# Optimization experiments

Hardware: AMD Instinct MI355X
Metric: run time of the kernel (lower is better)

Reference implementation:

```python
import jax, jax.numpy as jnp
import numpy as np

B, N, C, H = 4, 8192, 1024, 16
D = C // H

def setup_inputs() -> dict:
    key = jax.random.key(0)
    k1, k2, k3 = jax.random.split(key, 3)
    scale_in = 1.0 / np.sqrt(C)
    return {
        "x": jax.random.normal(k1, (B, N, C), dtype=jnp.float32),
        "w_qkv": jax.random.normal(k2, (C, 3 * C), dtype=jnp.float32) * scale_in,
        "b_qkv": jnp.zeros((3 * C,), dtype=jnp.float32),
        "w_proj": jax.random.normal(k3, (C, C), dtype=jnp.float32) * scale_in,
        "b_proj": jnp.zeros((C,), dtype=jnp.float32),
    }

def reference(x, w_qkv, b_qkv, w_proj, b_proj):
    Bx, Nx, Cx = x.shape
    qkv = x @ w_qkv + b_qkv                       # [B,N,3C]
    qkv = qkv.reshape(Bx, Nx, 3, H, D)
    qkv = jnp.transpose(qkv, (2, 0, 3, 1, 4))     # [3,B,H,N,D]
    q, k, v = qkv[0], qkv[1], qkv[2]
    q = jax.nn.elu(q) + 1.0                       # positive feature map
    k = jax.nn.elu(k) + 1.0
    kv = jnp.einsum('bhnd,bhne->bhde', k, v)      # [B,H,D,D]
    out = jnp.einsum('bhnd,bhde->bhne', q, kv)    # [B,H,N,D]
    z = 1.0 / (jnp.einsum('bhnd,bhd->bhn', q, k.sum(axis=2)) + 1e-8)
    out = out * z[..., None]
    out = jnp.transpose(out, (0, 2, 1, 3)).reshape(Bx, Nx, Cx)
    out = out @ w_proj + b_proj                   # dropout is identity in eval
    return out
```

## Files before the change

kernel.cpp:

```cpp
#include <hip/hip_runtime.h>
#include <hip/hip_bf16.h>
#include <stdint.h>

typedef unsigned short ushort_t;
typedef __attribute__((ext_vector_type(8))) short short8;
typedef __attribute__((ext_vector_type(4))) float floatx4;

__device__ __forceinline__ ushort_t f2b(float f) {
    unsigned u = __float_as_uint(f);
    unsigned r = (u + 0x7FFFu + ((u >> 16) & 1u)) >> 16;
    return (ushort_t)r;
}
__device__ __forceinline__ float b2f(ushort_t h) {
    return __uint_as_float(((unsigned)h) << 16);
}
__device__ __forceinline__ float elu1(float f) {
    return (f > 0.f) ? (f + 1.f) : __expf(f);
}

#define GLDS16(srcp, dstp)                                                          \
    __builtin_amdgcn_global_load_lds(                                               \
        (const __attribute__((address_space(1))) unsigned int*)(srcp),              \
        (__attribute__((address_space(3))) unsigned int*)(dstp), 16, 0, 0)


__global__ void conv_bf16(const float* __restrict__ in, ushort_t* __restrict__ out, int n8) {
    for (int i = blockIdx.x * blockDim.x + threadIdx.x; i < n8; i += gridDim.x * blockDim.x) {
        const float4 f0 = *(const float4*)&in[(size_t)i * 8];
        const float4 f1 = *(const float4*)&in[(size_t)i * 8 + 4];
        ushort4 o0, o1;
        o0.x = f2b(f0.x); o0.y = f2b(f0.y); o0.z = f2b(f0.z); o0.w = f2b(f0.w);
        o1.x = f2b(f1.x); o1.y = f2b(f1.y); o1.z = f2b(f1.z); o1.w = f2b(f1.w);
        *(ushort4*)&out[(size_t)i * 8]     = o0;
        *(ushort4*)&out[(size_t)i * 8 + 4] = o1;
    }
}

__global__ void transpose_conv(const float* __restrict__ in, ushort_t* __restrict__ out,
                               int R, int C) {
    __shared__ float tile[32][33];
    int c0 = blockIdx.x * 32, r0 = blockIdx.y * 32;
    int tx = threadIdx.x, ty = threadIdx.y;
#pragma unroll
    for (int k = 0; k < 4; ++k) {
        int a = ty * 4 + k;
        tile[a][tx] = in[(size_t)(r0 + a) * C + c0 + tx];
    }
    __syncthreads();
#pragma unroll
    for (int k = 0; k < 4; ++k) {
        int a = ty * 4 + k;
        out[(size_t)(c0 + a) * R + r0 + tx] = f2b(tile[tx][a]);
    }
}

__global__ void zero_f32(float* __restrict__ p, int n) {
    int i = blockIdx.x * blockDim.x + threadIdx.x;
    if (i < n) p[i] = 0.f;
}

template<int MODE>
__global__ __launch_bounds__(512, 2) void gemm256(
    const ushort_t* __restrict__ A, const ushort_t* __restrict__ Bt,
    const float* __restrict__ bias,
    ushort_t* __restrict__ out_u16, float* __restrict__ out_f32,
    int Nt, int nbx)
{
    extern __shared__ ushort_t lds[];
    constexpr int KK = 1024;

    const int tid  = threadIdx.x;
    const int wave = tid >> 6;
    const int lane = tid & 63;
    const int wm_i = wave >> 2;
    const int wn_i = wave & 3;
    const int fr   = lane & 15;
    const int fq   = lane >> 4;

    const int nwg = (int)gridDim.x;
    const int bid = (int)blockIdx.x;
    const int swz = (bid & 7) * (nwg >> 3) + (bid >> 3);
    const int bx = swz % nbx, by = swz / nbx;
    const int m0 = by * 256, n0 = bx * 256;

    const int trow = tid >> 3;
    const int csw  = ((tid & 7) ^ (trow & 7)) << 3;
    const int tcolB = ((tid >> 8) << 6) + (trow & 31);

    const ushort_t* sa = A  + (size_t)(m0 + trow)  * KK + csw;
    const ushort_t* sb = Bt + (size_t)(n0 + tcolB) * KK + csw;

    const int dstA = wave * 512;
    const int dstB = 16384 + wave * 512;

    const int sw0 = (fq ^ (fr & 7)) << 3;
    const int sw1 = sw0 ^ 32;
    const int abase = (wm_i * 64 + fr) * 64;
    const int bbase = (wn_i * 32 + fr) * 64;
    int loA0[2][2], loA1[2][2], loB0[2][2], loB1[2][2];
#pragma unroll
    for (int bf = 0; bf < 2; ++bf)
#pragma unroll
        for (int q = 0; q < 2; ++q) {
            loA0[bf][q] = bf * 32768 + q * 8192 + abase + sw0;
            loA1[bf][q] = bf * 32768 + q * 8192 + abase + sw1;
            loB0[bf][q] = bf * 32768 + 16384 + q * 8192 + bbase + sw0;
            loB1[bf][q] = bf * 32768 + 16384 + q * 8192 + bbase + sw1;
        }

    floatx4 acc[8][4];
    const floatx4 z4 = {0.f, 0.f, 0.f, 0.f};
#pragma unroll
    for (int i = 0; i < 8; ++i)
#pragma unroll
        for (int j = 0; j < 4; ++j) acc[i][j] = z4;

    short8 a[4][2], b[2][2];

    auto stageA = [&](int buf, int h, int ko) {
        ushort_t* d = lds + buf * 32768 + h * 8192 + dstA;
        GLDS16(sa + h * (64 * KK) + ko, d);
        GLDS16(sa + h * (64 * KK) + 128 * KK + ko, d + 4096);
    };
    auto stageB = [&](int buf, int h, int ko) {
        ushort_t* d = lds + buf * 32768 + h * 8192 + dstB;
        GLDS16(sb + h * (32 * KK) + ko, d);
        GLDS16(sb + h * (32 * KK) + 128 * KK + ko, d + 4096);
    };
    auto loadA = [&](int buf, int qr) {
        const int o0 = loA0[buf][qr], o1 = loA1[buf][qr];
#pragma unroll
        for (int i = 0; i < 4; ++i) {
            a[i][0] = *(const short8*)(lds + o0 + i * 1024);
            a[i][1] = *(const short8*)(lds + o1 + i * 1024);
        }
    };
    auto loadB = [&](int buf, int qc) {
        const int o0 = loB0[buf][qc], o1 = loB1[buf][qc];
#pragma unroll
        for (int j = 0; j < 2; ++j) {
            b[j][0] = *(const short8*)(lds + o0 + j * 1024);
            b[j][1] = *(const short8*)(lds + o1 + j * 1024);
        }
    };
    auto mma = [&](int qr, int qc) {
#pragma unroll
        for (int i = 0; i < 4; ++i)
#pragma unroll
            for (int j = 0; j < 2; ++j) {
                acc[qr * 4 + i][qc * 2 + j] =
                    __builtin_amdgcn_mfma_f32_16x16x32_bf16(b[j][0], a[i][0], acc[qr * 4 + i][qc * 2 + j], 0, 0, 0);
                acc[qr * 4 + i][qc * 2 + j] =
                    __builtin_amdgcn_mfma_f32_16x16x32_bf16(b[j][1], a[i][1], acc[qr * 4 + i][qc * 2 + j], 0, 0, 0);
            }
    };

#define PRIO1() __builtin_amdgcn_s_setprio(1)
#define BOUT()  __builtin_amdgcn_s_setprio(0); __builtin_amdgcn_s_barrier()
#define VM6()   asm volatile("s_waitcnt vmcnt(6)" ::: "memory")
#define VM0()   asm volatile("s_waitcnt vmcnt(0)" ::: "memory")

    stageA(0, 0, 0);
    stageB(0, 1, 0);
    stageA(0, 1, 0);
    stageB(0, 0, 0);
    stageA(1, 0, 64);
    stageB(1, 1, 64);
    stageA(1, 1, 64);
    VM6();
    __builtin_amdgcn_s_barrier();

    int ko = 0;
    for (int pr = 0; pr < 7; ++pr, ko += 128) {
        loadA(0, 0); loadB(0, 0);
        stageB(1, 0, ko + 64);
        PRIO1(); mma(0, 0); BOUT();

        loadB(0, 1);
        stageA(0, 0, ko + 128);
        PRIO1(); mma(0, 1); BOUT();

        loadA(0, 1);
        stageB(0, 1, ko + 128);
        PRIO1(); mma(1, 1); BOUT();

        loadB(0, 0);
        stageA(0, 1, ko + 128);
        PRIO1(); mma(1, 0); __builtin_amdgcn_s_setprio(0); VM6();
        __builtin_amdgcn_s_barrier();

        loadA(1, 0); loadB(1, 0);
        stageB(0, 0, ko + 128);
        PRIO1(); mma(0, 0); BOUT();

        loadB(1, 1);
        stageA(1, 0, ko + 192);
        PRIO1(); mma(0, 1); BOUT();

        loadA(1, 1);
        stageB(1, 1, ko + 192);
        PRIO1(); mma(1, 1); BOUT();

        loadB(1, 0);
        stageA(1, 1, ko + 192);
        PRIO1(); mma(1, 0); __builtin_amdgcn_s_setprio(0); VM6();
        __builtin_amdgcn_s_barrier();
    }

    loadA(0, 0); loadB(0, 0);
    stageB(1, 0, 960);
    PRIO1(); mma(0, 0); BOUT();

    loadB(0, 1);
    PRIO1(); mma(0, 1); BOUT();

    loadA(0, 1);
    PRIO1(); mma(1, 1); BOUT();

    loadB(0, 0);
    PRIO1(); mma(1, 0); __builtin_amdgcn_s_setprio(0); VM0();
    __builtin_amdgcn_s_barrier();

    loadA(1, 0); loadB(1, 0);
    PRIO1(); mma(0, 0); BOUT();

    loadB(1, 1);
    PRIO1(); mma(0, 1); BOUT();

    loadA(1, 1);
    PRIO1(); mma(1, 1); BOUT();

    loadB(1, 0);
    PRIO1(); mma(1, 0);
    __builtin_amdgcn_s_setprio(0);

#undef PRIO1
#undef BOUT
#undef VM6
#undef VM0

    float4 bv[4];
#pragma unroll
    for (int cj = 0; cj < 4; ++cj) {
        const int nb = n0 + wn_i * 64 + (cj >> 1) * 32 + (cj & 1) * 16 + fq * 4;
        bv[cj] = *(const float4*)&bias[nb];
    }
#pragma unroll
    for (int ri = 0; ri < 8; ++ri) {
        const int m = m0 + wm_i * 128 + (ri >> 2) * 64 + (ri & 3) * 16 + fr;
#pragma unroll
        for (int cj = 0; cj < 4; ++cj) {
            const int nb = n0 + wn_i * 64 + (cj >> 1) * 32 + (cj & 1) * 16 + fq * 4;
            if (MODE == 0) {
                ushort4 o;
                o.x = f2b(acc[ri][cj][0] + bv[cj].x);
                o.y = f2b(acc[ri][cj][1] + bv[cj].y);
                o.z = f2b(acc[ri][cj][2] + bv[cj].z);
                o.w = f2b(acc[ri][cj][3] + bv[cj].w);
                *(ushort4*)&out_u16[(size_t)m * Nt + nb] = o;
            } else {
                float4 o;
                o.x = acc[ri][cj][0] + bv[cj].x;
                o.y = acc[ri][cj][1] + bv[cj].y;
                o.z = acc[ri][cj][2] + bv[cj].z;
                o.w = acc[ri][cj][3] + bv[cj].w;
                *(float4*)&out_f32[(size_t)m * Nt + nb] = o;
            }
        }
    }
}

__global__ __launch_bounds__(256) void kv_kernel(
    const ushort_t* __restrict__ qkvb,
    float* __restrict__ kv, float* __restrict__ ksum)
{
    __shared__ ushort_t ks[64 * 64] __attribute__((aligned(16)));
    __shared__ ushort_t vs[64 * 64] __attribute__((aligned(16)));

    const int bh = blockIdx.y, chunk = blockIdx.x, t = threadIdx.x;
    const int b = bh >> 4, h = bh & 15;
    const int d0 = (t >> 4) * 4, e0 = (t & 15) * 4;
    const bool do_ksum = (t & 15) == 0;

    const int sr = t >> 2;
    const int sc = (t & 3) * 16;

    float acc[4][4];
#pragma unroll
    for (int i = 0; i < 4; ++i)
#pragma unroll
        for (int j = 0; j < 4; ++j) acc[i][j] = 0.f;
    float kacc[4] = {0.f, 0.f, 0.f, 0.f};

    for (int sub = 0; sub < 8; ++sub) {
        const int nb = chunk * 512 + sub * 64;
        __syncthreads();
        {
            const ushort_t* row = qkvb + ((size_t)b * 8192 + nb + sr) * 3072 + h * 64 + sc;
            short8 k0 = *(const short8*)(row + 1024);
            short8 k1 = *(const short8*)(row + 1024 + 8);
            short8 ko0, ko1;
#pragma unroll
            for (int i = 0; i < 8; ++i) {
                ko0[i] = (short)f2b(elu1(b2f((ushort_t)k0[i])));
                ko1[i] = (short)f2b(elu1(b2f((ushort_t)k1[i])));
            }
            *(short8*)&ks[sr * 64 + sc]     = ko0;
            *(short8*)&ks[sr * 64 + sc + 8] = ko1;
            *(short8*)&vs[sr * 64 + sc]     = *(const short8*)(row + 2048);
            *(short8*)&vs[sr * 64 + sc + 8] = *(const short8*)(row + 2048 + 8);
        }
        __syncthreads();
        for (int n = 0; n < 64; ++n) {
            ushort4 kd = *(const ushort4*)&ks[n * 64 + d0];
            ushort4 ve = *(const ushort4*)&vs[n * 64 + e0];
            float kf[4] = {b2f(kd.x), b2f(kd.y), b2f(kd.z), b2f(kd.w)};
            float vf[4] = {b2f(ve.x), b2f(ve.y), b2f(ve.z), b2f(ve.w)};
#pragma unroll
            for (int i = 0; i < 4; ++i) {
#pragma unroll
                for (int j = 0; j < 4; ++j) acc[i][j] += kf[i] * vf[j];
            }
            if (do_ksum) {
#pragma unroll
                for (int i = 0; i < 4; ++i) kacc[i] += kf[i];
            }
        }
    }
#pragma unroll
    for (int i = 0; i < 4; ++i) {
        if (do_ksum) atomicAdd(&ksum[bh * 64 + d0 + i], kacc[i]);
#pragma unroll
        for (int j = 0; j < 4; ++j)
            atomicAdd(&kv[((size_t)bh * 64 + d0 + i) * 64 + e0 + j], acc[i][j]);
    }
}

__global__ __launch_bounds__(256) void out_kernel(
    const ushort_t* __restrict__ qkvb, const float* __restrict__ kv,
    const float* __restrict__ ksum, ushort_t* __restrict__ obuf)
{
    __shared__ float kvs[4096];
    __shared__ float ksums[64];
    __shared__ float qs[16][65];

    const int bh = blockIdx.y, chunk = blockIdx.x, t = threadIdx.x;
    const int b = bh >> 4, h = bh & 15;
    const int myrow = t >> 4, e0 = (t & 15) * 4;

#pragma unroll
    for (int i = 0; i < 4; ++i) {
        int idx = (i * 256 + t) * 4;
        *(float4*)&kvs[idx] = *(const float4*)&kv[(size_t)bh * 4096 + idx];
    }
    if (t < 64) ksums[t] = ksum[bh * 64 + t];

    for (int pass = 0; pass < 8; ++pass) {
        const int n = chunk * 128 + pass * 16 + myrow;
        __syncthreads();
        {
            int col = (t & 15) * 4;
            ushort4 qv4 = *(const ushort4*)&qkvb[((size_t)b * 8192 + n) * 3072 + h * 64 + col];
            qs[myrow][col + 0] = elu1(b2f(qv4.x));
            qs[myrow][col + 1] = elu1(b2f(qv4.y));
            qs[myrow][col + 2] = elu1(b2f(qv4.z));
            qs[myrow][col + 3] = elu1(b2f(qv4.w));
        }
        __syncthreads();
        float a0 = 0.f, a1 = 0.f, a2 = 0.f, a3 = 0.f, z = 0.f;
        for (int d = 0; d < 64; ++d) {
            const float qv = qs[myrow][d];
            const float4 kvv = *(const float4*)&kvs[d * 64 + e0];
            a0 += qv * kvv.x; a1 += qv * kvv.y; a2 += qv * kvv.z; a3 += qv * kvv.w;
            z += qv * ksums[d];
        }
        const float zi = 1.f / (z + 1e-8f);
        ushort4 o;
        o.x = f2b(a0 * zi); o.y = f2b(a1 * zi); o.z = f2b(a2 * zi); o.w = f2b(a3 * zi);
        *(ushort4*)&obuf[((size_t)b * 8192 + n) * 1024 + h * 64 + e0] = o;
    }
}


extern "C" void kernel_launch(void* const* d_in, const int* in_sizes, int n_in,
                              void* d_out, int out_size, void* d_ws, size_t ws_size,
                              hipStream_t stream) {
    const float* x      = (const float*)d_in[0];
    const float* w_qkv  = (const float*)d_in[1];
    const float* b_qkv  = (const float*)d_in[2];
    const float* w_proj = (const float*)d_in[3];
    const float* b_proj = (const float*)d_in[4];
    float* out = (float*)d_out;

    const size_t XE = (size_t)32768 * 1024;

    char* ws = (char*)d_ws;
    ushort_t* xb   = (ushort_t*)ws;  ws += XE * 2;
    ushort_t* wqT  = (ushort_t*)ws;  ws += (size_t)3072 * 1024 * 2;
    ushort_t* wpT  = (ushort_t*)ws;  ws += (size_t)1024 * 1024 * 2;
    ushort_t* qkvb = (ushort_t*)ws;  ws += 3 * XE * 2;
    ushort_t* ob   = (ushort_t*)ws;  ws += XE * 2;
    float*    kv   = (float*)ws;     ws += (size_t)64 * 64 * 64 * 4;
    float*    ksum = (float*)ws;     ws += (size_t)64 * 64 * 4;

    (void)hipFuncSetAttribute(reinterpret_cast<const void*>(gemm256<0>),
                              hipFuncAttributeMaxDynamicSharedMemorySize, 131072);
    (void)hipFuncSetAttribute(reinterpret_cast<const void*>(gemm256<1>),
                              hipFuncAttributeMaxDynamicSharedMemorySize, 131072);

    zero_f32<<<dim3((64 * 64 * 64 + 64 * 64 + 255) / 256), dim3(256), 0, stream>>>(kv, 64 * 64 * 64 + 64 * 64);
    conv_bf16<<<dim3(2048), dim3(256), 0, stream>>>(x, xb, (int)(XE / 8));
    transpose_conv<<<dim3(96, 32), dim3(32, 8), 0, stream>>>(w_qkv, wqT, 1024, 3072);
    transpose_conv<<<dim3(32, 32), dim3(32, 8), 0, stream>>>(w_proj, wpT, 1024, 1024);

    gemm256<0><<<dim3(1536), dim3(512), 131072, stream>>>(xb, wqT, b_qkv, qkvb, nullptr, 3072, 12);

    kv_kernel<<<dim3(16, 64), dim3(256), 0, stream>>>(qkvb, kv, ksum);
    out_kernel<<<dim3(64, 64), dim3(256), 0, stream>>>(qkvb, kv, ksum, ob);

    gemm256<1><<<dim3(512), dim3(512), 131072, stream>>>(ob, wpT, b_proj, nullptr, out, 1024, 4);
}
```

Before: 559.9 us.

## Fuse ELU into QKV GEMM epilogue, write head-major layout, use MFMA in output kernel

The QKV GEMM epilogue now applies the elu+1 feature map to the Q and K columns and scatters results into a head-major [3,B,H,N,D] layout. The kv kernel can then do contiguous loads without per-element ELU. The output kernel is rewritten to compute q·kv and the normalizer with bf16 MFMA instructions, replacing the scalar LDS-based FMA loop, and uses fewer, larger blocks. Risks include scattered stores in the GEMM epilogue and extra bf16 rounding of kv and ksum.

```diff
diff --git a/kernel.cpp b/kernel.cpp
--- a/kernel.cpp
+++ b/kernel.cpp
@@ -250,40 +250,44 @@
         const int m = m0 + wm_i * 128 + (ri >> 2) * 64 + (ri & 3) * 16 + fr;
 #pragma unroll
         for (int cj = 0; cj < 4; ++cj) {
-            const int nb = n0 + wn_i * 64 + (cj >> 1) * 32 + (cj & 1) * 16 + fq * 4;
+            const int col = n0 + wn_i * 64 + (cj >> 1) * 32 + (cj & 1) * 16 + fq * 4;
             if (MODE == 0) {
+                const int s = col >> 10;
+                const int c = col & 1023;
+                const int h = c >> 6;
+                const int d = c & 63;
+                const int bb = m >> 13;
+                const int n  = m & 8191;
+                float v0 = acc[ri][cj][0] + bv[cj].x;
+                float v1 = acc[ri][cj][1] + bv[cj].y;
+                float v2 = acc[ri][cj][2] + bv[cj].z;
+                float v3 = acc[ri][cj][3] + bv[cj].w;
+                if (s < 2) { v0 = elu1(v0); v1 = elu1(v1); v2 = elu1(v2); v3 = elu1(v3); }
                 ushort4 o;
-                o.x = f2b(acc[ri][cj][0] + bv[cj].x);
-                o.y = f2b(acc[ri][cj][1] + bv[cj].y);
-                o.z = f2b(acc[ri][cj][2] + bv[cj].z);
-                o.w = f2b(acc[ri][cj][3] + bv[cj].w);
-                *(ushort4*)&out_u16[(size_t)m * Nt + nb] = o;
+                o.x = f2b(v0); o.y = f2b(v1); o.z = f2b(v2); o.w = f2b(v3);
+                *(ushort4*)&out_u16[(((size_t)s * 64 + bb * 16 + h) * 8192 + n) * 64 + d] = o;
             } else {
                 float4 o;
                 o.x = acc[ri][cj][0] + bv[cj].x;
                 o.y = acc[ri][cj][1] + bv[cj].y;
                 o.z = acc[ri][cj][2] + bv[cj].z;
                 o.w = acc[ri][cj][3] + bv[cj].w;
-                *(float4*)&out_f32[(size_t)m * Nt + nb] = o;
+                *(float4*)&out_f32[(size_t)m * Nt + col] = o;
             }
         }
     }
 }
 
 __global__ __launch_bounds__(256) void kv_kernel(
-    const ushort_t* __restrict__ qkvb,
+    const ushort_t* __restrict__ kbuf, const ushort_t* __restrict__ vbuf,
     float* __restrict__ kv, float* __restrict__ ksum)
 {
     __shared__ ushort_t ks[64 * 64] __attribute__((aligned(16)));
     __shared__ ushort_t vs[64 * 64] __attribute__((aligned(16)));
 
     const int bh = blockIdx.y, chunk = blockIdx.x, t = threadIdx.x;
-    const int b = bh >> 4, h = bh & 15;
     const int d0 = (t >> 4) * 4, e0 = (t & 15) * 4;
     const bool do_ksum = (t & 15) == 0;
-
-    const int sr = t >> 2;
-    const int sc = (t & 3) * 16;
 
     float acc[4][4];
 #pragma unroll
@@ -295,20 +299,12 @@
     for (int sub = 0; sub < 8; ++sub) {
         const int nb = chunk * 512 + sub * 64;
         __syncthreads();
-        {
-            const ushort_t* row = qkvb + ((size_t)b * 8192 + nb + sr) * 3072 + h * 64 + sc;
-            short8 k0 = *(const short8*)(row + 1024);
-            short8 k1 = *(const short8*)(row + 1024 + 8);
-            short8 ko0, ko1;
-#pragma unroll
-            for (int i = 0; i < 8; ++i) {
-                ko0[i] = (short)f2b(elu1(b2f((ushort_t)k0[i])));
-                ko1[i] = (short)f2b(elu1(b2f((ushort_t)k1[i])));
-            }
-            *(short8*)&ks[sr * 64 + sc]     = ko0;
-            *(short8*)&ks[sr * 64 + sc + 8] = ko1;
-            *(short8*)&vs[sr * 64 + sc]     = *(const short8*)(row + 2048);
-            *(short8*)&vs[sr * 64 + sc + 8] = *(const short8*)(row + 2048 + 8);
+#pragma unroll
+        for (int p = 0; p < 2; ++p) {
+            int idx = p * 256 + t;
+            int r = idx >> 3, c = (idx & 7) * 8;
+            *(short8*)&ks[r * 64 + c] = *(const short8*)&kbuf[((size_t)bh * 8192 + nb + r) * 64 + c];
+            *(short8*)&vs[r * 64 + c] = *(const short8*)&vbuf[((size_t)bh * 8192 + nb + r) * 64 + c];
         }
         __syncthreads();
         for (int n = 0; n < 64; ++n) {
@@ -337,16 +333,16 @@
 }
 
 __global__ __launch_bounds__(256) void out_kernel(
-    const ushort_t* __restrict__ qkvb, const float* __restrict__ kv,
+    const ushort_t* __restrict__ qbuf, const float* __restrict__ kv,
     const float* __restrict__ ksum, ushort_t* __restrict__ obuf)
 {
     __shared__ float kvs[4096];
     __shared__ float ksums[64];
-    __shared__ float qs[16][65];
 
     const int bh = blockIdx.y, chunk = blockIdx.x, t = threadIdx.x;
     const int b = bh >> 4, h = bh & 15;
-    const int myrow = t >> 4, e0 = (t & 15) * 4;
+    const int wave = t >> 6, lane = t & 63;
+    const int tok = lane & 15, fq = lane >> 4;
 
 #pragma unroll
     for (int i = 0; i < 4; ++i) {
@@ -354,30 +350,55 @@
         *(float4*)&kvs[idx] = *(const float4*)&kv[(size_t)bh * 4096 + idx];
     }
     if (t < 64) ksums[t] = ksum[bh * 64 + t];
-
-    for (int pass = 0; pass < 8; ++pass) {
-        const int n = chunk * 128 + pass * 16 + myrow;
-        __syncthreads();
-        {
-            int col = (t & 15) * 4;
-            ushort4 qv4 = *(const ushort4*)&qkvb[((size_t)b * 8192 + n) * 3072 + h * 64 + col];
-            qs[myrow][col + 0] = elu1(b2f(qv4.x));
-            qs[myrow][col + 1] = elu1(b2f(qv4.y));
-            qs[myrow][col + 2] = elu1(b2f(qv4.z));
-            qs[myrow][col + 3] = elu1(b2f(qv4.w));
-        }
-        __syncthreads();
-        float a0 = 0.f, a1 = 0.f, a2 = 0.f, a3 = 0.f, z = 0.f;
-        for (int d = 0; d < 64; ++d) {
-            const float qv = qs[myrow][d];
-            const float4 kvv = *(const float4*)&kvs[d * 64 + e0];
-            a0 += qv * kvv.x; a1 += qv * kvv.y; a2 += qv * kvv.z; a3 += qv * kvv.w;
-            z += qv * ksums[d];
-        }
-        const float zi = 1.f / (z + 1e-8f);
-        ushort4 o;
-        o.x = f2b(a0 * zi); o.y = f2b(a1 * zi); o.z = f2b(a2 * zi); o.w = f2b(a3 * zi);
-        *(ushort4*)&obuf[((size_t)b * 8192 + n) * 1024 + h * 64 + e0] = o;
+    __syncthreads();
+
+    short8 afr[4][2];
+#pragma unroll
+    for (int et = 0; et < 4; ++et)
+#pragma unroll
+        for (int kslice = 0; kslice < 2; ++kslice)
+#pragma unroll
+            for (int i = 0; i < 8; ++i) {
+                const int d = kslice * 32 + fq * 8 + i;
+                afr[et][kslice][i] = (short)f2b(kvs[d * 64 + et * 16 + tok]);
+            }
+    short8 zfr[2];
+#pragma unroll
+    for (int kslice = 0; kslice < 2; ++kslice)
+#pragma unroll
+        for (int i = 0; i < 8; ++i)
+            zfr[kslice][i] = (short)f2b(ksums[kslice * 32 + fq * 8 + i]);
+
+    const floatx4 z4 = {0.f, 0.f, 0.f, 0.f};
+    const int nbase = chunk * 1024 + wave * 256;
+    const ushort_t* qrow = qbuf + ((size_t)bh * 8192 + nbase + tok) * 64 + fq * 8;
+    ushort_t* orow = obuf + ((size_t)b * 8192 + nbase + tok) * 1024 + h * 64 + fq * 4;
+
+#pragma unroll 2
+    for (int g = 0; g < 16; ++g) {
+        short8 bf0 = *(const short8*)(qrow + (size_t)g * 16 * 64);
+        short8 bf1 = *(const short8*)(qrow + (size_t)g * 16 * 64 + 32);
+
+        floatx4 az = __builtin_amdgcn_mfma_f32_16x16x32_bf16(zfr[0], bf0, z4, 0, 0, 0);
+        az = __builtin_amdgcn_mfma_f32_16x16x32_bf16(zfr[1], bf1, az, 0, 0, 0);
+
+        floatx4 ad[4];
+#pragma unroll
+        for (int et = 0; et < 4; ++et) {
+            ad[et] = __builtin_amdgcn_mfma_f32_16x16x32_bf16(afr[et][0], bf0, z4, 0, 0, 0);
+            ad[et] = __builtin_amdgcn_mfma_f32_16x16x32_bf16(afr[et][1], bf1, ad[et], 0, 0, 0);
+        }
+
+        const float zi = 1.f / (az[0] + 1e-8f);
+#pragma unroll
+        for (int et = 0; et < 4; ++et) {
+            ushort4 o;
+            o.x = f2b(ad[et][0] * zi);
+            o.y = f2b(ad[et][1] * zi);
+            o.z = f2b(ad[et][2] * zi);
+            o.w = f2b(ad[et][3] * zi);
+            *(ushort4*)&orow[(size_t)g * 16 * 1024 + et * 16] = o;
+        }
     }
 }
 
@@ -415,8 +436,8 @@
 
     gemm256<0><<<dim3(1536), dim3(512), 131072, stream>>>(xb, wqT, b_qkv, qkvb, nullptr, 3072, 12);
 
-    kv_kernel<<<dim3(16, 64), dim3(256), 0, stream>>>(qkvb, kv, ksum);
-    out_kernel<<<dim3(64, 64), dim3(256), 0, stream>>>(qkvb, kv, ksum, ob);
+    kv_kernel<<<dim3(16, 64), dim3(256), 0, stream>>>(qkvb + XE, qkvb + 2 * XE, kv, ksum);
+    out_kernel<<<dim3(8, 64), dim3(256), 0, stream>>>(qkvb, kv, ksum, ob);
 
     gemm256<1><<<dim3(512), dim3(512), 131072, stream>>>(ob, wpT, b_proj, nullptr, out, 1024, 4);
 }
```

New measurement: 490.3 us. -12.4%, faster.
